# Kernel tuning notes

Measured on AMD Instinct MI355X. Metric: run time of the kernel, lower is better.

The kernel has to match this reference:

```python
import jax, jax.numpy as jnp
import numpy as np

B, C, H, W = 16, 256, 32, 32
NH = 4
GROUPS = 8
EPS = 1e-5


def setup_inputs() -> dict:
    key = jax.random.key(0)
    ks = jax.random.split(key, 7)
    x = jax.random.normal(ks[0], (B, C, H, W), dtype=jnp.float32)
    norm_w = jnp.ones((C,), jnp.float32)
    norm_b = jnp.zeros((C,), jnp.float32)
    # 1x1 convs == per-pixel linear maps; store as [out, in] matrices
    qkv_w = jax.random.normal(ks[1], (3 * C, C), dtype=jnp.float32) * (1.0 / np.sqrt(C))
    qkv_b = jnp.zeros((3 * C,), jnp.float32)
    proj_w = jax.random.normal(ks[2], (C, C), dtype=jnp.float32) * (1.0 / np.sqrt(C))
    proj_b = jnp.zeros((C,), jnp.float32)
    return {"x": x, "norm_w": norm_w, "norm_b": norm_b,
            "qkv_w": qkv_w, "qkv_b": qkv_b, "proj_w": proj_w, "proj_b": proj_b}


def _group_norm(x, w, b):
    # x: [B, C, H, W], GROUPS groups over channel dim
    b_, c, h, w_ = x.shape
    xg = x.reshape(b_, GROUPS, c // GROUPS, h, w_)
    mean = xg.mean(axis=(2, 3, 4), keepdims=True)
    var = xg.var(axis=(2, 3, 4), keepdims=True)
    xg = (xg - mean) * jax.lax.rsqrt(var + EPS)
    x = xg.reshape(b_, c, h, w_)
    return x * w[None, :, None, None] + b[None, :, None, None]


def reference(x, norm_w, norm_b, qkv_w, qkv_b, proj_w, proj_b):
    b, c, h, w = x.shape
    nh, d = NH, c // NH
    s = h * w
    hn = _group_norm(x, norm_w, norm_b)
    # 1x1 conv: [3C, C] x [B, C, S] -> [B, 3C, S]
    hf = hn.reshape(b, c, s)
    qkv = jnp.einsum('oc,bcs->bos', qkv_w, hf) + qkv_b[None, :, None]
    # channel layout: (t h d); -> [B, 3, nh, d, S] -> per-tensor [B, nh, S, d]
    qkv = qkv.reshape(b, 3, nh, d, s)
    q = jnp.transpose(qkv[:, 0], (0, 1, 3, 2))  # [B, nh, S, d]
    k = jnp.transpose(qkv[:, 1], (0, 1, 3, 2))
    v = jnp.transpose(qkv[:, 2], (0, 1, 3, 2))
    scale = 1.0 / np.sqrt(d).astype(np.float32)
    attn = jnp.einsum('bhqd,bhkd->bhqk', q, k) * scale
    attn = jax.nn.softmax(attn, axis=-1)
    out = jnp.einsum('bhqk,bhkd->bhqd', attn, v)        # [B, nh, S, d]
    out = jnp.transpose(out, (0, 1, 3, 2)).reshape(b, c, s)  # b (h d) s
    out = jnp.einsum('oc,bcs->bos', proj_w, out) + proj_b[None, :, None]
    return x + out.reshape(b, c, h, w)
```

## Files before the change

kernel.cpp:

```cpp
#include <hip/hip_runtime.h>

#define NB 16
#define NC 256
#define NS 1024
#define NNH 4
#define ND 64
#define GN_EPS 1e-5f

typedef __attribute__((ext_vector_type(8))) short short8;
typedef __attribute__((ext_vector_type(4))) float f32x4;

static __device__ __forceinline__ ushort f2bf(float x) {
  union { float f; unsigned u; } c; c.f = x;
  unsigned r = (c.u + 0x7fffu + ((c.u >> 16) & 1u)) >> 16;
  return (ushort)r;
}
static __device__ __forceinline__ unsigned cvt_pk_bf16(float lo, float hi) {
  unsigned r;
  asm("v_cvt_pk_bf16_f32 %0, %1, %2" : "=v"(r) : "v"(lo), "v"(hi));
  return r;
}

__global__ __launch_bounds__(256) void gnstat_wconv_kernel(
    const float* __restrict__ x, float2* __restrict__ partials,
    const float* __restrict__ qw, const float* __restrict__ pw,
    ushort* __restrict__ wbf) {
  const int bid = blockIdx.x;
  const int t = threadIdx.x;
  if (bid >= 1024) {
    const int i = (bid - 1024) * 256 + t;
    const float4 v = (i < 49152) ? *(const float4*)(qw + (size_t)i * 4)
                                 : *(const float4*)(pw + (size_t)(i - 49152) * 4);
    ushort4 u;
    u.x = f2bf(v.x); u.y = f2bf(v.y); u.z = f2bf(v.z); u.w = f2bf(v.w);
    *(ushort4*)(wbf + (size_t)i * 4) = u;
    return;
  }
  const int bg = bid >> 3, part = bid & 7;
  const float4* xv = (const float4*)(x + (size_t)bg * 32768 + part * 4096);
  float s1 = 0.f, s2 = 0.f;
  #pragma unroll
  for (int i = 0; i < 4; ++i) {
    float4 v = xv[t + 256 * i];
    s1 += v.x + v.y + v.z + v.w;
    s2 += v.x * v.x + v.y * v.y + v.z * v.z + v.w * v.w;
  }
  #pragma unroll
  for (int o = 32; o > 0; o >>= 1) {
    s1 += __shfl_down(s1, o, 64);
    s2 += __shfl_down(s2, o, 64);
  }
  __shared__ float rs1[4], rs2[4];
  const int wid = t >> 6;
  if ((t & 63) == 0) { rs1[wid] = s1; rs2[wid] = s2; }
  __syncthreads();
  if (t == 0) {
    partials[bg * 8 + part] = make_float2(rs1[0] + rs1[1] + rs1[2] + rs1[3],
                                          rs2[0] + rs2[1] + rs2[2] + rs2[3]);
  }
}

__global__ __launch_bounds__(256) void gnapply_kernel(
    const float* __restrict__ x, const float* __restrict__ nw,
    const float* __restrict__ nb, const float2* __restrict__ partials,
    ushort* __restrict__ hnT) {
  const int bid = blockIdx.x;
  const int bg = bid >> 3, st = bid & 7;
  const int b = bg >> 3, gg = bg & 7;
  const int t = threadIdx.x;

  float s1 = 0.f, s2 = 0.f;
  #pragma unroll
  for (int j = 0; j < 8; ++j) {
    const float2 p = partials[bg * 8 + j];
    s1 += p.x; s2 += p.y;
  }
  const float mean = s1 * (1.f / 32768.f);
  const float var = s2 * (1.f / 32768.f) - mean * mean;
  const float rstd = rsqrtf(var + GN_EPS);

  __shared__ ushort tile[128][36];
  const int s4 = (t & 31) * 4;
  #pragma unroll
  for (int i = 0; i < 4; ++i) {
    const int c = (t >> 5) + 8 * i;
    const int cg = gg * 32 + c;
    const float wgt = nw[cg] * rstd;
    const float bia = nb[cg] - mean * wgt;
    const float4 v = *(const float4*)(x + ((size_t)(b * NC + cg)) * NS +
                                      st * 128 + s4);
    tile[s4 + 0][c] = f2bf(v.x * wgt + bia);
    tile[s4 + 1][c] = f2bf(v.y * wgt + bia);
    tile[s4 + 2][c] = f2bf(v.z * wgt + bia);
    tile[s4 + 3][c] = f2bf(v.w * wgt + bia);
  }
  __syncthreads();
  #pragma unroll
  for (int i = 0; i < 4; ++i) {
    const int idx = t + 256 * i;
    const int sr = idx >> 3, ch4 = (idx & 7) * 4;
    const ushort4 u = *(const ushort4*)&tile[sr][ch4];
    *(ushort4*)(hnT + ((size_t)(b * NS + st * 128 + sr)) * NC + gg * 32 + ch4) = u;
  }
}

template <int EPI, int YDIM>
__global__ __launch_bounds__(256) void mfma_gemm_kernel(
    const ushort* __restrict__ Wbf, const float* __restrict__ bias,
    const ushort* __restrict__ DATA, const float* __restrict__ X,
    ushort* __restrict__ qT, ushort* __restrict__ kT, ushort* __restrict__ vN,
    float* __restrict__ OUT) {
  __shared__ char smem[32768];
  char* T1 = smem;
  char* T2 = smem + 16384;
  const int nwg = 8 * YDIM * NB;
  const int o_id = blockIdx.x;
  const int wg = (o_id & 7) * (nwg >> 3) + (o_id >> 3);
  const int b = wg / (8 * YDIM);
  const int o0 = ((wg >> 3) % YDIM) * 128, s0 = (wg & 7) * 128;
  const int t = threadIdx.x, w = t >> 6, l = t & 63;
  const int g = l >> 4, li = l & 15;
  const ushort* wrow = Wbf + (size_t)o0 * NC;
  const ushort* drow = DATA + ((size_t)b * NS + s0) * NC;

  f32x4 acc[4][4];
  #pragma unroll
  for (int i = 0; i < 4; ++i)
    #pragma unroll
    for (int j = 0; j < 4; ++j) acc[i][j] = (f32x4){0.f, 0.f, 0.f, 0.f};

  const int oh = (w >> 1) * 64, sh = (w & 1) * 64;

  for (int k0 = 0; k0 < NC; k0 += 64) {
    short8 r1[4], r2[4];
    #pragma unroll
    for (int i = 0; i < 4; ++i) {
      const int id = t + 256 * i, row = id >> 3, ce = (id & 7) * 8;
      r1[i] = *(const short8*)(wrow + (size_t)row * NC + k0 + ce);
      r2[i] = *(const short8*)(drow + (size_t)row * NC + k0 + ce);
    }
    __syncthreads();
    #pragma unroll
    for (int i = 0; i < 4; ++i) {
      const int id = t + 256 * i, row = id >> 3, cb = (id & 7) * 16;
      const int dst = row * 128 + (cb ^ ((row & 7) << 4));
      *(short8*)(T1 + dst) = r1[i];
      *(short8*)(T2 + dst) = r2[i];
    }
    __syncthreads();
    __builtin_amdgcn_s_setprio(1);
    #pragma unroll
    for (int kk = 0; kk < 2; ++kk) {
      short8 af[4], bfr[4];
      #pragma unroll
      for (int ms = 0; ms < 4; ++ms) {
        const int row = oh + ms * 16 + li;
        af[ms] = *(const short8*)(T1 + row * 128 +
                                  ((kk * 64 + g * 16) ^ ((row & 7) << 4)));
      }
      #pragma unroll
      for (int ns = 0; ns < 4; ++ns) {
        const int row = sh + ns * 16 + li;
        bfr[ns] = *(const short8*)(T2 + row * 128 +
                                   ((kk * 64 + g * 16) ^ ((row & 7) << 4)));
      }
      #pragma unroll
      for (int ms = 0; ms < 4; ++ms)
        #pragma unroll
        for (int ns = 0; ns < 4; ++ns)
          acc[ms][ns] = __builtin_amdgcn_mfma_f32_16x16x32_bf16(
              af[ms], bfr[ns], acc[ms][ns], 0, 0, 0);
    }
    __builtin_amdgcn_s_setprio(0);
  }

  const int ob = o0 + oh;
  if (EPI == 0) {
    const int tsr = ob >> 8;
    const int h = (ob >> 6) & 3;
    if (tsr < 2) {
      const float sc = (tsr == 0) ? 0.18033688f : 1.0f;
      ushort* dst = (tsr == 0 ? qT : kT) + ((size_t)(b * 4 + h)) * NS * ND;
      #pragma unroll
      for (int ms = 0; ms < 4; ++ms) {
        const float4 bv = *(const float4*)(bias + ob + ms * 16 + g * 4);
        const int d0 = ms * 16 + g * 4;
        #pragma unroll
        for (int ns = 0; ns < 4; ++ns) {
          const int s = s0 + sh + ns * 16 + li;
          ushort4 pk;
          pk.x = f2bf((acc[ms][ns][0] + bv.x) * sc);
          pk.y = f2bf((acc[ms][ns][1] + bv.y) * sc);
          pk.z = f2bf((acc[ms][ns][2] + bv.z) * sc);
          pk.w = f2bf((acc[ms][ns][3] + bv.w) * sc);
          *(ushort4*)(dst + (size_t)s * ND + d0) = pk;
        }
      }
    } else {
      ushort* dst = vN + ((size_t)(b * 4 + h)) * ND * NS;
      #pragma unroll
      for (int ms = 0; ms < 4; ++ms) {
        const float4 bv = *(const float4*)(bias + ob + ms * 16 + g * 4);
        const float bvr[4] = {bv.x, bv.y, bv.z, bv.w};
        #pragma unroll
        for (int r = 0; r < 4; ++r) {
          const int d = ms * 16 + g * 4 + r;
          #pragma unroll
          for (int ns = 0; ns < 4; ++ns) {
            const int s = s0 + sh + ns * 16 + li;
            dst[(size_t)d * NS + s] = f2bf(acc[ms][ns][r] + bvr[r]);
          }
        }
      }
    }
  } else {
    float* outb = OUT + (size_t)b * NC * NS;
    const float* xb = X + (size_t)b * NC * NS;
    #pragma unroll
    for (int ms = 0; ms < 4; ++ms) {
      const float4 bv = *(const float4*)(bias + ob + ms * 16 + g * 4);
      const float bvr[4] = {bv.x, bv.y, bv.z, bv.w};
      #pragma unroll
      for (int r = 0; r < 4; ++r) {
        const int c = ob + ms * 16 + g * 4 + r;
        #pragma unroll
        for (int ns = 0; ns < 4; ++ns) {
          const int s = s0 + sh + ns * 16 + li;
          const size_t a = (size_t)c * NS + s;
          outb[a] = acc[ms][ns][r] + bvr[r] + xb[a];
        }
      }
    }
  }
}

__global__ __launch_bounds__(512, 2) void attn_kernel(
    const ushort* __restrict__ qT, const ushort* __restrict__ kT,
    const ushort* __restrict__ vN, ushort* __restrict__ att2) {
  __shared__ char smem[65536];
  const int o_id = blockIdx.x;
  const int wg = (o_id & 7) * 32 + (o_id >> 3);
  const int b = wg >> 4, h = (wg >> 2) & 3;
  const int sq0 = (wg & 3) * 256;
  const int t = threadIdx.x, w = t >> 6, l = t & 63;
  const int g = l >> 4, li = l & 15;
  const int sw = (li & 7) << 4;
  char* Ps = smem + 32768 + w * 4096;
  const size_t bh = (size_t)(b * 4 + h);
  const ushort* qbase = qT + bh * NS * ND + (size_t)sq0 * ND;
  const ushort* kbase = kT + bh * NS * ND;
  const ushort* vbase = vN + bh * ND * NS;

  #pragma unroll
  for (int i = 0; i < 4; ++i) {
    const int f = t + 512 * i;
    const int row = f >> 3, c8 = f & 7;
    short8 v = *(const short8*)(qbase + (size_t)row * ND + c8 * 8);
    *(short8*)(smem + 32768 + ((row * 128 + c8 * 16) ^ ((row & 7) << 4))) = v;
  }
  __syncthreads();
  short8 aq[2][2];
  #pragma unroll
  for (int m = 0; m < 2; ++m) {
    const int row = w * 32 + m * 16 + li;
    aq[m][0] = *(const short8*)(smem + 32768 + row * 128 + ((g * 16) ^ sw));
    aq[m][1] = *(const short8*)(smem + 32768 + row * 128 + ((64 + g * 16) ^ sw));
  }

  const int srow = t >> 3, sc8 = t & 7;
  const int sdst = srow * 128 + ((sc8 * 16) ^ ((srow & 7) << 4));
  {
    short8 k0 = *(const short8*)(kbase + (size_t)srow * ND + sc8 * 8);
    short8 v0 = *(const short8*)(vbase + (size_t)srow * NS + sc8 * 8);
    *(short8*)(smem + sdst) = k0;
    *(short8*)(smem + 8192 + sdst) = v0;
  }

  f32x4 acc[2][4];
  #pragma unroll
  for (int m = 0; m < 2; ++m)
    #pragma unroll
    for (int dt = 0; dt < 4; ++dt) acc[m][dt] = (f32x4){0.f, 0.f, 0.f, 0.f};
  float lsum[2] = {0.f, 0.f};

  for (int kt = 0; kt < 16; ++kt) {
    __syncthreads();
    char* Kc = smem + (kt & 1) * 16384;
    char* Vc = Kc + 8192;

    short8 nk, nv;
    if (kt < 15) {
      nk = *(const short8*)(kbase + (size_t)(kt + 1) * 64 * ND +
                            (size_t)srow * ND + sc8 * 8);
      nv = *(const short8*)(vbase + (size_t)srow * NS + (kt + 1) * 64 + sc8 * 8);
    }

    __builtin_amdgcn_s_setprio(1);
    #pragma unroll
    for (int kst = 0; kst < 4; ++kst) {
      const int krow = kst * 16 + li;
      const short8 bk0 = *(const short8*)(Kc + krow * 128 + ((g * 16) ^ sw));
      const short8 bk1 = *(const short8*)(Kc + krow * 128 + ((64 + g * 16) ^ sw));
      #pragma unroll
      for (int m = 0; m < 2; ++m) {
        f32x4 sT = {0.f, 0.f, 0.f, 0.f};
        sT = __builtin_amdgcn_mfma_f32_16x16x32_bf16(bk0, aq[m][0], sT, 0, 0, 0);
        sT = __builtin_amdgcn_mfma_f32_16x16x32_bf16(bk1, aq[m][1], sT, 0, 0, 0);
        const float p0 = __builtin_amdgcn_exp2f(sT[0]);
        const float p1 = __builtin_amdgcn_exp2f(sT[1]);
        const float p2 = __builtin_amdgcn_exp2f(sT[2]);
        const float p3 = __builtin_amdgcn_exp2f(sT[3]);
        lsum[m] += (p0 + p1) + (p2 + p3);
        uint2 pk;
        pk.x = cvt_pk_bf16(p0, p1);
        pk.y = cvt_pk_bf16(p2, p3);
        *(uint2*)(Ps + (m * 16 + li) * 128 + ((kst * 32 + 8 * g) ^ sw)) = pk;
      }
    }
    __builtin_amdgcn_s_setprio(0);

    __builtin_amdgcn_s_setprio(1);
    #pragma unroll
    for (int ks2 = 0; ks2 < 2; ++ks2) {
      short8 pa[2];
      #pragma unroll
      for (int m = 0; m < 2; ++m)
        pa[m] = *(const short8*)(Ps + (m * 16 + li) * 128 +
                                 ((ks2 * 64 + g * 16) ^ sw));
      #pragma unroll
      for (int dt = 0; dt < 4; ++dt) {
        const int vrow = dt * 16 + li;
        const short8 bv = *(const short8*)(Vc + vrow * 128 +
                                           ((ks2 * 64 + g * 16) ^ sw));
        #pragma unroll
        for (int m = 0; m < 2; ++m)
          acc[m][dt] = __builtin_amdgcn_mfma_f32_16x16x32_bf16(
              pa[m], bv, acc[m][dt], 0, 0, 0);
      }
    }
    __builtin_amdgcn_s_setprio(0);

    if (kt < 15) {
      char* Kn = smem + ((kt + 1) & 1) * 16384;
      *(short8*)(Kn + sdst) = nk;
      *(short8*)(Kn + 8192 + sdst) = nv;
    }
  }

  float lr[2][4];
  #pragma unroll
  for (int m = 0; m < 2; ++m) {
    float s = lsum[m];
    s += __shfl_xor(s, 16, 64);
    s += __shfl_xor(s, 32, 64);
    const float linv = 1.f / s;
    #pragma unroll
    for (int r = 0; r < 4; ++r) lr[m][r] = __shfl(linv, g * 4 + r, 64);
  }

  ushort* obase = att2 + ((size_t)b * NS + sq0 + w * 32) * NC + h * 64;
  #pragma unroll
  for (int m = 0; m < 2; ++m)
    #pragma unroll
    for (int dt = 0; dt < 4; ++dt)
      #pragma unroll
      for (int r = 0; r < 4; ++r)
        obase[(size_t)(m * 16 + g * 4 + r) * NC + dt * 16 + li] =
            f2bf(acc[m][dt][r] * lr[m][r]);
}

extern "C" void kernel_launch(void* const* d_in, const int* in_sizes, int n_in,
                              void* d_out, int out_size, void* d_ws, size_t ws_size,
                              hipStream_t stream) {
  const float* x      = (const float*)d_in[0];
  const float* norm_w = (const float*)d_in[1];
  const float* norm_b = (const float*)d_in[2];
  const float* qkv_w  = (const float*)d_in[3];
  const float* qkv_b  = (const float*)d_in[4];
  const float* proj_w = (const float*)d_in[5];
  const float* proj_b = (const float*)d_in[6];
  float* out = (float*)d_out;

  ushort* hnT  = (ushort*)d_ws;
  ushort* qT   = hnT + (size_t)4194304;
  ushort* kT   = qT + (size_t)4194304;
  ushort* vN   = kT + (size_t)4194304;
  ushort* att2 = vN + (size_t)4194304;
  ushort* wbf  = att2 + (size_t)4194304;
  float2* partials = (float2*)(wbf + (size_t)262144);
  ushort* wq = wbf;
  ushort* wp = wbf + (size_t)196608;

  gnstat_wconv_kernel<<<dim3(1280), 256, 0, stream>>>(
      x, partials, qkv_w, proj_w, wbf);
  gnapply_kernel<<<dim3(1024), 256, 0, stream>>>(
      x, norm_w, norm_b, partials, hnT);
  mfma_gemm_kernel<0, 6><<<dim3(768), 256, 0, stream>>>(
      wq, qkv_b, hnT, nullptr, qT, kT, vN, nullptr);
  attn_kernel<<<dim3(256), 512, 0, stream>>>(qT, kT, vN, att2);
  mfma_gemm_kernel<1, 2><<<dim3(256), 256, 0, stream>>>(
      wp, proj_b, att2, x, nullptr, nullptr, nullptr, out);
}
```

Before: 61.31 us.

## Fold group-norm affine into per-batch QKV weights to read x once

The GroupNorm scale and shift are folded into per-batch copies of the QKV weight matrix and bias. The first pass over x can then compute the statistics and write the transposed bf16 copy of raw x together, so the separate apply pass that re-read x is gone. A small kernel builds 16 scaled bf16 weight sets plus adjusted biases. In exchange the QKV GEMM reads per-batch weights (larger weight footprint), and casting raw x to bf16 before normalising may change rounding slightly.

```diff
diff --git a/kernel.cpp b/kernel.cpp
--- a/kernel.cpp
+++ b/kernel.cpp
@@ -21,87 +21,103 @@
   return r;
 }
 
-__global__ __launch_bounds__(256) void gnstat_wconv_kernel(
-    const float* __restrict__ x, float2* __restrict__ partials,
-    const float* __restrict__ qw, const float* __restrict__ pw,
-    ushort* __restrict__ wbf) {
-  const int bid = blockIdx.x;
-  const int t = threadIdx.x;
-  if (bid >= 1024) {
-    const int i = (bid - 1024) * 256 + t;
-    const float4 v = (i < 49152) ? *(const float4*)(qw + (size_t)i * 4)
-                                 : *(const float4*)(pw + (size_t)(i - 49152) * 4);
-    ushort4 u;
-    u.x = f2bf(v.x); u.y = f2bf(v.y); u.z = f2bf(v.z); u.w = f2bf(v.w);
-    *(ushort4*)(wbf + (size_t)i * 4) = u;
-    return;
-  }
-  const int bg = bid >> 3, part = bid & 7;
-  const float4* xv = (const float4*)(x + (size_t)bg * 32768 + part * 4096);
-  float s1 = 0.f, s2 = 0.f;
-  #pragma unroll
-  for (int i = 0; i < 4; ++i) {
-    float4 v = xv[t + 256 * i];
-    s1 += v.x + v.y + v.z + v.w;
-    s2 += v.x * v.x + v.y * v.y + v.z * v.z + v.w * v.w;
-  }
-  #pragma unroll
-  for (int o = 32; o > 0; o >>= 1) {
-    s1 += __shfl_down(s1, o, 64);
-    s2 += __shfl_down(s2, o, 64);
-  }
-  __shared__ float rs1[4], rs2[4];
-  const int wid = t >> 6;
-  if ((t & 63) == 0) { rs1[wid] = s1; rs2[wid] = s2; }
-  __syncthreads();
-  if (t == 0) {
-    partials[bg * 8 + part] = make_float2(rs1[0] + rs1[1] + rs1[2] + rs1[3],
-                                          rs2[0] + rs2[1] + rs2[2] + rs2[3]);
-  }
-}
-
-__global__ __launch_bounds__(256) void gnapply_kernel(
-    const float* __restrict__ x, const float* __restrict__ nw,
-    const float* __restrict__ nb, const float2* __restrict__ partials,
-    ushort* __restrict__ hnT) {
+__global__ __launch_bounds__(256) void gnstatT_kernel(
+    const float* __restrict__ x, ushort* __restrict__ xT,
+    float2* __restrict__ partials) {
   const int bid = blockIdx.x;
   const int bg = bid >> 3, st = bid & 7;
   const int b = bg >> 3, gg = bg & 7;
   const int t = threadIdx.x;
 
+  __shared__ ushort tile[128][36];
+  __shared__ float rs1[4], rs2[4];
+  const int s4 = (t & 31) * 4;
   float s1 = 0.f, s2 = 0.f;
-  #pragma unroll
-  for (int j = 0; j < 8; ++j) {
-    const float2 p = partials[bg * 8 + j];
-    s1 += p.x; s2 += p.y;
-  }
-  const float mean = s1 * (1.f / 32768.f);
-  const float var = s2 * (1.f / 32768.f) - mean * mean;
-  const float rstd = rsqrtf(var + GN_EPS);
-
-  __shared__ ushort tile[128][36];
-  const int s4 = (t & 31) * 4;
   #pragma unroll
   for (int i = 0; i < 4; ++i) {
     const int c = (t >> 5) + 8 * i;
     const int cg = gg * 32 + c;
-    const float wgt = nw[cg] * rstd;
-    const float bia = nb[cg] - mean * wgt;
     const float4 v = *(const float4*)(x + ((size_t)(b * NC + cg)) * NS +
                                       st * 128 + s4);
-    tile[s4 + 0][c] = f2bf(v.x * wgt + bia);
-    tile[s4 + 1][c] = f2bf(v.y * wgt + bia);
-    tile[s4 + 2][c] = f2bf(v.z * wgt + bia);
-    tile[s4 + 3][c] = f2bf(v.w * wgt + bia);
-  }
+    s1 += v.x + v.y + v.z + v.w;
+    s2 += v.x * v.x + v.y * v.y + v.z * v.z + v.w * v.w;
+    tile[s4 + 0][c] = f2bf(v.x);
+    tile[s4 + 1][c] = f2bf(v.y);
+    tile[s4 + 2][c] = f2bf(v.z);
+    tile[s4 + 3][c] = f2bf(v.w);
+  }
+  #pragma unroll
+  for (int o = 32; o > 0; o >>= 1) {
+    s1 += __shfl_down(s1, o, 64);
+    s2 += __shfl_down(s2, o, 64);
+  }
+  if ((t & 63) == 0) { rs1[t >> 6] = s1; rs2[t >> 6] = s2; }
   __syncthreads();
+  if (t == 0)
+    partials[bid] = make_float2(rs1[0] + rs1[1] + rs1[2] + rs1[3],
+                                rs2[0] + rs2[1] + rs2[2] + rs2[3]);
   #pragma unroll
   for (int i = 0; i < 4; ++i) {
     const int idx = t + 256 * i;
     const int sr = idx >> 3, ch4 = (idx & 7) * 4;
     const ushort4 u = *(const ushort4*)&tile[sr][ch4];
-    *(ushort4*)(hnT + ((size_t)(b * NS + st * 128 + sr)) * NC + gg * 32 + ch4) = u;
-  }
+    *(ushort4*)(xT + ((size_t)(b * NS + st * 128 + sr)) * NC + gg * 32 + ch4) = u;
+  }
+}
+
+__global__ __launch_bounds__(256) void wprep_kernel(
+    const float* __restrict__ qw, const float* __restrict__ qb,
+    const float* __restrict__ pw, const float* __restrict__ nw,
+    const float* __restrict__ nb, const float2* __restrict__ partials,
+    ushort* __restrict__ wq, float* __restrict__ biasq,
+    ushort* __restrict__ wp) {
+  const int bid = blockIdx.x;
+  const int t = threadIdx.x;
+  if (bid >= 192) {
+    const int i = (bid - 192) * 256 + t;
+    const float4 v = *(const float4*)(pw + (size_t)i * 4);
+    ushort4 u;
+    u.x = f2bf(v.x); u.y = f2bf(v.y); u.z = f2bf(v.z); u.w = f2bf(v.w);
+    *(ushort4*)(wp + (size_t)i * 4) = u;
+    return;
+  }
+  const int b = bid / 12, o0 = (bid % 12) * 64;
+  __shared__ float2 sm_g[8];
+  __shared__ float2 sm_wb[256];
+  if (t < 8) {
+    float s1 = 0.f, s2 = 0.f;
+    #pragma unroll
+    for (int j = 0; j < 8; ++j) {
+      const float2 p = partials[(b * 8 + t) * 8 + j];
+      s1 += p.x; s2 += p.y;
+    }
+    const float mean = s1 * (1.f / 32768.f);
+    const float var = s2 * (1.f / 32768.f) - mean * mean;
+    sm_g[t] = make_float2(mean, rsqrtf(var + GN_EPS));
+  }
+  __syncthreads();
+  {
+    const float2 ms = sm_g[t >> 5];
+    const float wgt = nw[t] * ms.y;
+    sm_wb[t] = make_float2(wgt, nb[t] - ms.x * wgt);
+  }
+  __syncthreads();
+  const int o = o0 + (t >> 2), c0 = (t & 3) * 64;
+  float dsum = 0.f;
+  for (int cc = 0; cc < 64; cc += 4) {
+    const int c = c0 + cc;
+    const float4 wv = *(const float4*)(qw + (size_t)o * NC + c);
+    const float2 wb0 = sm_wb[c + 0], wb1 = sm_wb[c + 1];
+    const float2 wb2 = sm_wb[c + 2], wb3 = sm_wb[c + 3];
+    dsum += wv.x * wb0.y + wv.y * wb1.y + wv.z * wb2.y + wv.w * wb3.y;
+    ushort4 u;
+    u.x = f2bf(wv.x * wb0.x); u.y = f2bf(wv.y * wb1.x);
+    u.z = f2bf(wv.z * wb2.x); u.w = f2bf(wv.w * wb3.x);
+    *(ushort4*)(wq + ((size_t)(b * 768) + o) * NC + c) = u;
+  }
+  dsum += __shfl_xor(dsum, 1, 64);
+  dsum += __shfl_xor(dsum, 2, 64);
+  if ((t & 3) == 0) biasq[b * 768 + o] = qb[o] + dsum;
 }
 
 template <int EPI, int YDIM>
@@ -120,7 +136,9 @@
   const int o0 = ((wg >> 3) % YDIM) * 128, s0 = (wg & 7) * 128;
   const int t = threadIdx.x, w = t >> 6, l = t & 63;
   const int g = l >> 4, li = l & 15;
-  const ushort* wrow = Wbf + (size_t)o0 * NC;
+  const ushort* wrow = Wbf + (EPI == 0 ? ((size_t)b * 768 + o0) * NC
+                                       : (size_t)o0 * NC);
+  const float* biasb = (EPI == 0) ? bias + b * 768 : bias;
   const ushort* drow = DATA + ((size_t)b * NS + s0) * NC;
 
   f32x4 acc[4][4];
@@ -183,7 +201,7 @@
       ushort* dst = (tsr == 0 ? qT : kT) + ((size_t)(b * 4 + h)) * NS * ND;
       #pragma unroll
       for (int ms = 0; ms < 4; ++ms) {
-        const float4 bv = *(const float4*)(bias + ob + ms * 16 + g * 4);
+        const float4 bv = *(const float4*)(biasb + ob + ms * 16 + g * 4);
         const int d0 = ms * 16 + g * 4;
         #pragma unroll
         for (int ns = 0; ns < 4; ++ns) {
@@ -200,7 +218,7 @@
       ushort* dst = vN + ((size_t)(b * 4 + h)) * ND * NS;
       #pragma unroll
       for (int ms = 0; ms < 4; ++ms) {
-        const float4 bv = *(const float4*)(bias + ob + ms * 16 + g * 4);
+        const float4 bv = *(const float4*)(biasb + ob + ms * 16 + g * 4);
         const float bvr[4] = {bv.x, bv.y, bv.z, bv.w};
         #pragma unroll
         for (int r = 0; r < 4; ++r) {
@@ -218,7 +236,7 @@
     const float* xb = X + (size_t)b * NC * NS;
     #pragma unroll
     for (int ms = 0; ms < 4; ++ms) {
-      const float4 bv = *(const float4*)(bias + ob + ms * 16 + g * 4);
+      const float4 bv = *(const float4*)(biasb + ob + ms * 16 + g * 4);
       const float bvr[4] = {bv.x, bv.y, bv.z, bv.w};
       #pragma unroll
       for (int r = 0; r < 4; ++r) {
@@ -381,22 +399,21 @@
   const float* proj_b = (const float*)d_in[6];
   float* out = (float*)d_out;
 
-  ushort* hnT  = (ushort*)d_ws;
-  ushort* qT   = hnT + (size_t)4194304;
+  ushort* xT   = (ushort*)d_ws;
+  ushort* qT   = xT + (size_t)4194304;
   ushort* kT   = qT + (size_t)4194304;
   ushort* vN   = kT + (size_t)4194304;
   ushort* att2 = vN + (size_t)4194304;
-  ushort* wbf  = att2 + (size_t)4194304;
-  float2* partials = (float2*)(wbf + (size_t)262144);
-  ushort* wq = wbf;
-  ushort* wp = wbf + (size_t)196608;
-
-  gnstat_wconv_kernel<<<dim3(1280), 256, 0, stream>>>(
-      x, partials, qkv_w, proj_w, wbf);
-  gnapply_kernel<<<dim3(1024), 256, 0, stream>>>(
-      x, norm_w, norm_b, partials, hnT);
+  ushort* wq   = att2 + (size_t)4194304;
+  ushort* wp   = wq + (size_t)3145728;
+  float* biasq = (float*)(wp + (size_t)65536);
+  float2* partials = (float2*)(biasq + 12288);
+
+  gnstatT_kernel<<<dim3(1024), 256, 0, stream>>>(x, xT, partials);
+  wprep_kernel<<<dim3(256), 256, 0, stream>>>(
+      qkv_w, qkv_b, proj_w, norm_w, norm_b, partials, wq, biasq, wp);
   mfma_gemm_kernel<0, 6><<<dim3(768), 256, 0, stream>>>(
-      wq, qkv_b, hnT, nullptr, qT, kT, vN, nullptr);
+      wq, biasq, xT, nullptr, qT, kT, vN, nullptr);
   attn_kernel<<<dim3(256), 512, 0, stream>>>(qT, kT, vN, att2);
   mfma_gemm_kernel<1, 2><<<dim3(256), 256, 0, stream>>>(
       wp, proj_b, att2, x, nullptr, nullptr, nullptr, out);
```

After: 64.62 us. 1.05x slower.
